# Optimization experiments

Hardware: AMD Instinct MI355X
Metric: run time of the kernel (lower is better)

Reference implementation:

```python
import jax, jax.numpy as jnp
import numpy as np

B, C, S = 32, 24, 7          # batch, feature channels, spatial side
N = S * S                    # 49 objects
Q = 2472                     # question vector dim (2524 - 2*(C+2))
RN = 256                     # rn_size


def _coords():
    # coord_tensor: [N, 2], ([i//7, i%7]) / 6
    i = jnp.arange(N)
    return jnp.stack([i // S, i % S], axis=1).astype(jnp.float32) / (S - 1)


def setup_inputs() -> dict:
    key = jax.random.key(0)
    ks = jax.random.split(key, 8)
    sc = lambda fan_in: 1.0 / np.sqrt(fan_in)
    return {
        "x":   jax.random.normal(ks[0], (B, C, S, S), dtype=jnp.float32),
        "qst": jax.random.normal(ks[1], (B, Q), dtype=jnp.float32),
        "W1":  jax.random.normal(ks[2], (2 * (C + 2) + Q, RN), dtype=jnp.float32) * sc(2524),
        "b1":  jax.random.normal(ks[3], (RN,), dtype=jnp.float32) * sc(2524),
        "Wg":  jax.random.normal(ks[4], (RN, RN), dtype=jnp.float32) * sc(RN),
        "bg":  jax.random.normal(ks[5], (RN,), dtype=jnp.float32) * sc(RN),
        "Wf":  jax.random.normal(ks[6], (RN, RN), dtype=jnp.float32) * sc(RN),
        "bf":  jax.random.normal(ks[7], (RN,), dtype=jnp.float32) * sc(RN),
        "g_layers": 2,
        "f_layers": 2,
    }


def reference(x, qst, W1, b1, Wg, bg, Wf, bf, g_layers, f_layers):
    mb = x.shape[0]
    # [B, C, 7, 7] -> [B, N, C], then append 2-d coords -> [B, N, C+2]
    x_flat = x.reshape(mb, C, N).transpose(0, 2, 1)
    coord = jnp.broadcast_to(_coords()[None], (mb, N, 2))
    x_flat = jnp.concatenate([x_flat, coord], axis=2)            # [B, N, D], D = C+2
    D = x_flat.shape[-1]

    # x_i[:, p, q, :] = x_flat[:, q, :]
    x_i = jnp.broadcast_to(x_flat[:, None, :, :], (mb, N, N, D))
    # x_j[:, p, q, :] = concat(x_flat[:, p, :], qst)
    xj_feat = jnp.concatenate(
        [x_flat, jnp.broadcast_to(qst[:, None, :], (mb, N, Q))], axis=2)  # [B, N, D+Q]
    x_j = jnp.broadcast_to(xj_feat[:, :, None, :], (mb, N, N, D + Q))
    x_full = jnp.concatenate([x_i, x_j], axis=3)                 # [B, N, N, 2D+Q]

    # g: shared edge MLP (note: ModuleList([Linear]*n) shares one weight)
    h = jax.nn.relu(jnp.einsum('bpqd,dr->bpqr', x_full, W1) + b1)
    for _ in range(g_layers):
        h = jax.nn.relu(jnp.einsum('bpqr,rs->bpqs', h, Wg) + bg)
    x_g = h.sum(axis=(1, 2))                                     # [B, RN]

    # f MLP (also shared weight across its layers)
    x_f = x_g
    for _ in range(f_layers):
        x_f = jax.nn.relu(x_f @ Wf + bf)
    return x_f
```

## Files before the change

### kernel.cpp

```cpp
#include <hip/hip_runtime.h>

#define BB 32
#define CC 24
#define SSIDE 7
#define NN 49
#define DD 26
#define QQ 2472
#define RN 256
#define NPQ 2401
#define BM 64
#define NT2 38

typedef float  f32x4  __attribute__((ext_vector_type(4)));
typedef short  short8 __attribute__((ext_vector_type(8)));
typedef __bf16 bfv8   __attribute__((ext_vector_type(8)));

#define QV_OFF   0
#define A2_OFF   65536
#define BJ_OFF   (A2_OFF + BB*NN*RN)
#define WGT_OFF  (BJ_OFF + BB*NN*RN)
#define PART_OFF (WGT_OFF + 32768)

static __device__ __forceinline__ short f2bf(float f) {
    return __builtin_bit_cast(short, (__bf16)f);
}

__global__ void k_qv_partial(const float* __restrict__ qst,
                             const float* __restrict__ W1,
                             float* __restrict__ ws) {
    const int b = blockIdx.x, j = blockIdx.y, r = threadIdx.x;
    const int KCH = QQ / 8;
    const int k0 = j * KCH;
    const float* q = qst + b * QQ + k0;
    const float* w = W1 + (2 * DD + k0) * RN + r;
    float acc = 0.f;
    #pragma unroll 4
    for (int k = 0; k < KCH; ++k)
        acc += q[k] * w[k * RN];
    ws[QV_OFF + (b * 8 + j) * RN + r] = acc;
}

__global__ void k_build_abj(const float* __restrict__ x,
                            const float* __restrict__ W1,
                            const float* __restrict__ b1,
                            float* __restrict__ ws) {
    const int ny = blockIdx.x, b = blockIdx.y, r = threadIdx.x;
    float qv = b1[r];
    #pragma unroll
    for (int j = 0; j < 8; ++j)
        qv += ws[QV_OFF + (b * 8 + j) * RN + r];

    for (int i = 0; i < 7; ++i) {
        const int n = ny * 7 + i;
        float a2 = 0.f, bj = 0.f;
        #pragma unroll
        for (int d = 0; d < DD; ++d) {
            float xv;
            if (d < CC)            xv = x[(b * CC + d) * NN + n];
            else if (d == CC)      xv = (float)(n / SSIDE) * (1.0f / 6.0f);
            else                   xv = (float)(n % SSIDE) * (1.0f / 6.0f);
            a2 += xv * W1[d * RN + r];
            bj += xv * W1[(DD + d) * RN + r];
        }
        ws[A2_OFF + (b * NN + n) * RN + r] = a2;
        ws[BJ_OFF + (b * NN + n) * RN + r] = bj + qv;
    }
}

__global__ void k_wgt(const float* __restrict__ Wg, float* __restrict__ ws) {
    const int n = blockIdx.x, k = threadIdx.x;
    short* wgt = (short*)(ws + WGT_OFF);
    wgt[n * RN + k] = f2bf(Wg[k * RN + n]);
}

__global__ __launch_bounds__(256) void k_g_mfma(const float* __restrict__ bg,
                                                float* __restrict__ ws) {
    const int bx = blockIdx.x, b = blockIdx.y;
    const int tid = threadIdx.x;
    const int lane = tid & 63, w = tid >> 6;
    const int lo = lane & 15, hi = lane >> 4;
    const int brow0 = bx * BM;
    const float* A2 = ws + A2_OFF + b * NN * RN;
    const float* Bj = ws + BJ_OFF + b * NN * RN;
    const short* wgt = (const short*)(ws + WGT_OFF);

    __shared__ short8 hbuf[BM * 32];
    short* hb = (short*)hbuf;

    #pragma unroll
    for (int it = 0; it < 8; ++it) {
        const int cid = it * 256 + tid;
        const int row = cid >> 5, chunk = cid & 31;
        const int grow = brow0 + row;
        short8 v8 = (short8)0;
        if (grow < NPQ) {
            const int p = grow / NN, q = grow - p * NN;
            const float4 a0 = *(const float4*)(A2 + q * RN + chunk * 8);
            const float4 a1 = *(const float4*)(A2 + q * RN + chunk * 8 + 4);
            const float4 b0 = *(const float4*)(Bj + p * RN + chunk * 8);
            const float4 b1v = *(const float4*)(Bj + p * RN + chunk * 8 + 4);
            v8[0] = f2bf(fmaxf(a0.x + b0.x, 0.f));
            v8[1] = f2bf(fmaxf(a0.y + b0.y, 0.f));
            v8[2] = f2bf(fmaxf(a0.z + b0.z, 0.f));
            v8[3] = f2bf(fmaxf(a0.w + b0.w, 0.f));
            v8[4] = f2bf(fmaxf(a1.x + b1v.x, 0.f));
            v8[5] = f2bf(fmaxf(a1.y + b1v.y, 0.f));
            v8[6] = f2bf(fmaxf(a1.z + b1v.z, 0.f));
            v8[7] = f2bf(fmaxf(a1.w + b1v.w, 0.f));
        }
        hbuf[row * 32 + (chunk ^ (row & 7))] = v8;
    }

    const int wcol0 = w * 64;
    bfv8 bfr[4][8];
    #pragma unroll
    for (int ct = 0; ct < 4; ++ct) {
        const int n = wcol0 + ct * 16 + lo;
        #pragma unroll
        for (int ks = 0; ks < 8; ++ks)
            bfr[ct][ks] = __builtin_bit_cast(bfv8,
                *(const short8*)(wgt + n * RN + ks * 32 + hi * 8));
    }
    float bgv[4];
    #pragma unroll
    for (int ct = 0; ct < 4; ++ct)
        bgv[ct] = bg[wcol0 + ct * 16 + lo];

    __syncthreads();

    f32x4 acc[4][4];

    #pragma unroll
    for (int ct = 0; ct < 4; ++ct)
        #pragma unroll
        for (int rt = 0; rt < 4; ++rt)
            acc[ct][rt] = (f32x4){0.f, 0.f, 0.f, 0.f};
    #pragma unroll
    for (int rt = 0; rt < 4; ++rt) {
        const int row = rt * 16 + lo;
        bfv8 afr[8];
        #pragma unroll
        for (int ks = 0; ks < 8; ++ks)
            afr[ks] = __builtin_bit_cast(bfv8,
                hbuf[row * 32 + ((ks * 4 + hi) ^ (row & 7))]);
        #pragma unroll
        for (int ct = 0; ct < 4; ++ct)
            #pragma unroll
            for (int ks = 0; ks < 8; ++ks)
                acc[ct][rt] = __builtin_amdgcn_mfma_f32_16x16x32_bf16(
                    afr[ks], bfr[ct][ks], acc[ct][rt], 0, 0, 0);
    }

    __syncthreads();
    #pragma unroll
    for (int ct = 0; ct < 4; ++ct) {
        const int n = wcol0 + ct * 16 + lo;
        #pragma unroll
        for (int rt = 0; rt < 4; ++rt) {
            #pragma unroll
            for (int r = 0; r < 4; ++r) {
                const int row = rt * 16 + hi * 4 + r;
                const float v = fmaxf(acc[ct][rt][r] + bgv[ct], 0.f);
                hb[row * 256 + (((n >> 3) ^ (row & 7)) << 3) + (n & 7)] = f2bf(v);
            }
        }
    }
    __syncthreads();

    #pragma unroll
    for (int ct = 0; ct < 4; ++ct)
        #pragma unroll
        for (int rt = 0; rt < 4; ++rt)
            acc[ct][rt] = (f32x4){0.f, 0.f, 0.f, 0.f};
    #pragma unroll
    for (int rt = 0; rt < 4; ++rt) {
        const int row = rt * 16 + lo;
        bfv8 afr[8];
        #pragma unroll
        for (int ks = 0; ks < 8; ++ks)
            afr[ks] = __builtin_bit_cast(bfv8,
                hbuf[row * 32 + ((ks * 4 + hi) ^ (row & 7))]);
        #pragma unroll
        for (int ct = 0; ct < 4; ++ct)
            #pragma unroll
            for (int ks = 0; ks < 8; ++ks)
                acc[ct][rt] = __builtin_amdgcn_mfma_f32_16x16x32_bf16(
                    afr[ks], bfr[ct][ks], acc[ct][rt], 0, 0, 0);
    }

    float cs[4] = {0.f, 0.f, 0.f, 0.f};
    #pragma unroll
    for (int ct = 0; ct < 4; ++ct) {
        #pragma unroll
        for (int rt = 0; rt < 4; ++rt) {
            #pragma unroll
            for (int r = 0; r < 4; ++r) {
                const int grow = brow0 + rt * 16 + hi * 4 + r;
                const float v = fmaxf(acc[ct][rt][r] + bgv[ct], 0.f);
                cs[ct] += (grow < NPQ) ? v : 0.f;
            }
        }
    }
    #pragma unroll
    for (int ct = 0; ct < 4; ++ct) {
        float v = cs[ct];
        v += __shfl_xor(v, 16);
        v += __shfl_xor(v, 32);
        if (hi == 0)
            ws[PART_OFF + (b * NT2 + bx) * RN + wcol0 + ct * 16 + lo] = v;
    }
}

__global__ void k_f_reduce(const float* __restrict__ Wf,
                           const float* __restrict__ bf,
                           const float* __restrict__ ws,
                           float* __restrict__ out) {
    const int b = blockIdx.x, r = threadIdx.x;
    __shared__ float xs[RN];
    float xg = 0.f;
    for (int t = 0; t < NT2; ++t)
        xg += ws[PART_OFF + (b * NT2 + t) * RN + r];
    xs[r] = xg;
    __syncthreads();

    float v = 0.f;
    #pragma unroll
    for (int layer = 0; layer < 2; ++layer) {
        float acc = bf[r];
        for (int s = 0; s < RN; ++s)
            acc += xs[s] * Wf[s * RN + r];
        v = fmaxf(acc, 0.f);
        __syncthreads();
        xs[r] = v;
        __syncthreads();
    }
    out[b * RN + r] = v;
}

extern "C" void kernel_launch(void* const* d_in, const int* in_sizes, int n_in,
                              void* d_out, int out_size, void* d_ws, size_t ws_size,
                              hipStream_t stream) {
    const float* x   = (const float*)d_in[0];
    const float* qst = (const float*)d_in[1];
    const float* W1  = (const float*)d_in[2];
    const float* b1  = (const float*)d_in[3];
    const float* Wg  = (const float*)d_in[4];
    const float* bg  = (const float*)d_in[5];
    const float* Wf  = (const float*)d_in[6];
    const float* bf  = (const float*)d_in[7];
    float* out = (float*)d_out;
    float* ws  = (float*)d_ws;

    k_qv_partial<<<dim3(BB, 8), RN, 0, stream>>>(qst, W1, ws);
    k_build_abj <<<dim3(7, BB), RN, 0, stream>>>(x, W1, b1, ws);
    k_wgt       <<<RN, RN, 0, stream>>>(Wg, ws);
    k_g_mfma    <<<dim3(NT2, BB), RN, 0, stream>>>(bg, ws);
    k_f_reduce  <<<BB, RN, 0, stream>>>(Wf, bf, ws, out);
}
```

Before: 177.2 us.

## Merge prep kernels, split qst GEMV finer and parallelize build per object

The question-vector GEMV is split into 24 K-chunks instead of 8, and the bf16 transpose of Wg now runs in the same launch through a tiled LDS transpose rather than a strided per-element kernel. The A2/Bj build kernel now uses one block per object instead of one per seven objects, giving more blocks. The aim is to fix low occupancy in the small preprocessing kernels and drop one launch. In exchange, the build step sums 24 partials instead of 8 per block and reloads the W1 rows once per object.

```diff
diff --git a/kernel.cpp b/kernel.cpp
--- a/kernel.cpp
+++ b/kernel.cpp
@@ -10,67 +10,80 @@
 #define NPQ 2401
 #define BM 64
 #define NT2 38
+#define NJ 24
+#define KCH 103
 
 typedef float  f32x4  __attribute__((ext_vector_type(4)));
 typedef short  short8 __attribute__((ext_vector_type(8)));
 typedef __bf16 bfv8   __attribute__((ext_vector_type(8)));
 
-#define QV_OFF   0
-#define A2_OFF   65536
+#define A2_OFF   0
 #define BJ_OFF   (A2_OFF + BB*NN*RN)
 #define WGT_OFF  (BJ_OFF + BB*NN*RN)
 #define PART_OFF (WGT_OFF + 32768)
+#define QV_OFF   PART_OFF
 
 static __device__ __forceinline__ short f2bf(float f) {
     return __builtin_bit_cast(short, (__bf16)f);
 }
 
-__global__ void k_qv_partial(const float* __restrict__ qst,
-                             const float* __restrict__ W1,
-                             float* __restrict__ ws) {
-    const int b = blockIdx.x, j = blockIdx.y, r = threadIdx.x;
-    const int KCH = QQ / 8;
-    const int k0 = j * KCH;
-    const float* q = qst + b * QQ + k0;
-    const float* w = W1 + (2 * DD + k0) * RN + r;
-    float acc = 0.f;
+__global__ __launch_bounds__(256) void k_prep(const float* __restrict__ qst,
+                                              const float* __restrict__ W1,
+                                              const float* __restrict__ Wg,
+                                              float* __restrict__ ws) {
+    const int bid = blockIdx.x;
+    if (bid < BB * NJ) {
+        const int b = bid / NJ, j = bid % NJ, r = threadIdx.x;
+        const int k0 = j * KCH;
+        const float* q = qst + b * QQ + k0;
+        const float* w = W1 + (2 * DD + k0) * RN + r;
+        float acc = 0.f;
+        #pragma unroll 4
+        for (int k = 0; k < KCH; ++k)
+            acc += q[k] * w[k * RN];
+        ws[QV_OFF + (b * NJ + j) * RN + r] = acc;
+    } else {
+        const int t = bid - BB * NJ;
+        const int kt = (t >> 2) * 64, nt = (t & 3) * 64;
+        const int tx = threadIdx.x & 63, ty = threadIdx.x >> 6;
+        __shared__ short lds[64 * 65];
+        short* wgt = (short*)(ws + WGT_OFF);
+        #pragma unroll
+        for (int i = 0; i < 16; ++i) {
+            const int k = ty + i * 4;
+            lds[tx * 65 + k] = f2bf(Wg[(kt + k) * RN + nt + tx]);
+        }
+        __syncthreads();
+        #pragma unroll
+        for (int i = 0; i < 16; ++i) {
+            const int n = ty + i * 4;
+            wgt[(nt + n) * RN + kt + tx] = lds[n * 65 + tx];
+        }
+    }
+}
+
+__global__ __launch_bounds__(256) void k_build_abj(const float* __restrict__ x,
+                                                   const float* __restrict__ W1,
+                                                   const float* __restrict__ b1,
+                                                   float* __restrict__ ws) {
+    const int n = blockIdx.x, b = blockIdx.y, r = threadIdx.x;
+    float qv = b1[r];
     #pragma unroll 4
-    for (int k = 0; k < KCH; ++k)
-        acc += q[k] * w[k * RN];
-    ws[QV_OFF + (b * 8 + j) * RN + r] = acc;
-}
-
-__global__ void k_build_abj(const float* __restrict__ x,
-                            const float* __restrict__ W1,
-                            const float* __restrict__ b1,
-                            float* __restrict__ ws) {
-    const int ny = blockIdx.x, b = blockIdx.y, r = threadIdx.x;
-    float qv = b1[r];
-    #pragma unroll
-    for (int j = 0; j < 8; ++j)
-        qv += ws[QV_OFF + (b * 8 + j) * RN + r];
-
-    for (int i = 0; i < 7; ++i) {
-        const int n = ny * 7 + i;
-        float a2 = 0.f, bj = 0.f;
-        #pragma unroll
-        for (int d = 0; d < DD; ++d) {
-            float xv;
-            if (d < CC)            xv = x[(b * CC + d) * NN + n];
-            else if (d == CC)      xv = (float)(n / SSIDE) * (1.0f / 6.0f);
-            else                   xv = (float)(n % SSIDE) * (1.0f / 6.0f);
-            a2 += xv * W1[d * RN + r];
-            bj += xv * W1[(DD + d) * RN + r];
-        }
-        ws[A2_OFF + (b * NN + n) * RN + r] = a2;
-        ws[BJ_OFF + (b * NN + n) * RN + r] = bj + qv;
-    }
-}
-
-__global__ void k_wgt(const float* __restrict__ Wg, float* __restrict__ ws) {
-    const int n = blockIdx.x, k = threadIdx.x;
-    short* wgt = (short*)(ws + WGT_OFF);
-    wgt[n * RN + k] = f2bf(Wg[k * RN + n]);
+    for (int j = 0; j < NJ; ++j)
+        qv += ws[QV_OFF + (b * NJ + j) * RN + r];
+
+    float a2 = 0.f, bj = 0.f;
+    #pragma unroll
+    for (int d = 0; d < DD; ++d) {
+        float xv;
+        if (d < CC)            xv = x[(b * CC + d) * NN + n];
+        else if (d == CC)      xv = (float)(n / SSIDE) * (1.0f / 6.0f);
+        else                   xv = (float)(n % SSIDE) * (1.0f / 6.0f);
+        a2 += xv * W1[d * RN + r];
+        bj += xv * W1[(DD + d) * RN + r];
+    }
+    ws[A2_OFF + (b * NN + n) * RN + r] = a2;
+    ws[BJ_OFF + (b * NN + n) * RN + r] = bj + qv;
 }
 
 __global__ __launch_bounds__(256) void k_g_mfma(const float* __restrict__ bg,
@@ -251,9 +264,8 @@
     float* out = (float*)d_out;
     float* ws  = (float*)d_ws;
 
-    k_qv_partial<<<dim3(BB, 8), RN, 0, stream>>>(qst, W1, ws);
-    k_build_abj <<<dim3(7, BB), RN, 0, stream>>>(x, W1, b1, ws);
-    k_wgt       <<<RN, RN, 0, stream>>>(Wg, ws);
+    k_prep      <<<BB * NJ + 16, RN, 0, stream>>>(qst, W1, Wg, ws);
+    k_build_abj <<<dim3(NN, BB), RN, 0, stream>>>(x, W1, b1, ws);
     k_g_mfma    <<<dim3(NT2, BB), RN, 0, stream>>>(bg, ws);
     k_f_reduce  <<<BB, RN, 0, stream>>>(Wf, bf, ws, out);
 }
```

After: 150.0 us. -15.3%, faster.
